# Optimization experiments

Measured on AMD Instinct MI355X. Metric: run time of the kernel, lower is better.

Reference implementation:

```python
import jax, jax.numpy as jnp
import numpy as np

# static module config (matches init_kwargs)
DIM = 128
HEADS = 8
DW, HW, WW = 5, 7, 7  # depth/height/width window


def _neighbor_indices(D, H, W):
    """Flat circular-neighborhood indices, shape (P, n) with P=D*H*W, n=DW*HW*WW."""
    od = np.arange(DW) - (DW - 1) // 2
    oh = np.arange(HW) - (HW - 1) // 2
    ow = np.arange(WW) - (WW - 1) // 2
    dd = (np.arange(D)[:, None] + od[None, :]) % D   # (D, DW)
    hh = (np.arange(H)[:, None] + oh[None, :]) % H   # (H, HW)
    ww = (np.arange(W)[:, None] + ow[None, :]) % W   # (W, WW)
    idx = (dd[:, None, None, :, None, None] * (H * W)
           + hh[None, :, None, None, :, None] * W
           + ww[None, None, :, None, None, :])        # (D,H,W,DW,HW,WW)
    return jnp.asarray(idx.reshape(D * H * W, DW * HW * WW), dtype=jnp.int32)


def setup_inputs() -> dict:
    key = jax.random.key(0)
    k1, k2, k3, k4, k5 = jax.random.split(key, 5)
    B, D, H, W, C = 1, 5, 24, 48, DIM
    w_scale = 1.0 / np.sqrt(C)  # keep attention logits in a sane range
    return {
        "x": jax.random.normal(k1, (B, D, H, W, C), dtype=jnp.float32),
        "qkv_w": jax.random.normal(k2, (3 * C, C), dtype=jnp.float32) * w_scale,
        "qkv_b": jax.random.normal(k3, (3 * C,), dtype=jnp.float32) * 0.01,
        "proj_w": jax.random.normal(k4, (C, C), dtype=jnp.float32) * w_scale,
        "proj_b": jax.random.normal(k5, (C,), dtype=jnp.float32) * 0.01,
    }


def reference(x, qkv_w, qkv_b, proj_w, proj_b):
    B, D, H, W, C = x.shape
    P = D * H * W
    n = DW * HW * WW
    hd = C // HEADS
    scale = hd ** -0.5
    idx = _neighbor_indices(D, H, W)                      # (P, n) int32, static

    xf = x.reshape(B, P, C)
    qkv = xf @ qkv_w.T + qkv_b                            # (B, P, 3C)
    q, k, v = jnp.split(qkv, 3, axis=-1)

    q = q.reshape(B, P, HEADS, hd)                        # center-pixel query
    k_g = k[:, idx].reshape(B, P, n, HEADS, hd)           # gathered circular neighborhood
    v_g = v[:, idx].reshape(B, P, n, HEADS, hd)

    scores = jnp.einsum('bphd,bpnhd->bhpn', q, k_g) * scale
    attn = jax.nn.softmax(scores, axis=-1)                # softmax over 245 neighbors
    out = jnp.einsum('bhpn,bpnhd->bphd', attn, v_g).reshape(B, P, C)
    out = out @ proj_w.T + proj_b
    return out.reshape(B, D, H, W, C)
```

## Files before the change

kernel.cpp:

```cpp
#include <hip/hip_runtime.h>
#include <hip/hip_bf16.h>
#include <cstddef>

#define DIMC   128
#define NHEADS 8
#define HDIM   16
#define DD     5
#define HH     24
#define WW_    48
#define NPOS   (DD * HH * WW_)
#define SCALE  0.25f

typedef short  bf16x8 __attribute__((ext_vector_type(8)));
typedef float  f32x4  __attribute__((ext_vector_type(4)));

__device__ __forceinline__ unsigned short f2bf(float f) {
    unsigned u = __float_as_uint(f);
    u = (u + 0x7FFFu + ((u >> 16) & 1u)) >> 16;
    return (unsigned short)u;
}
__device__ __forceinline__ float bf2f(unsigned short s) {
    return __uint_as_float(((unsigned)s) << 16);
}

__global__ __launch_bounds__(256, 3) void gemm_qkv_kernel(
    const float* __restrict__ x,
    const float* __restrict__ wq,
    const float* __restrict__ qkv_b,
    unsigned short* __restrict__ Qhl,
    unsigned short* __restrict__ Kbf,
    unsigned short* __restrict__ Vbf)
{
    __shared__ __align__(16) unsigned short Bs[64][264];

    const int tid = threadIdx.x;
    const int bn  = blockIdx.x * 64;
    const int bm  = blockIdx.y * 64;

    for (int i = tid; i < 2048; i += 256) {
        const int r = i >> 5, c4 = (i & 31) * 4;
        const float4 v = *(const float4*)(wq + (size_t)(bn + r) * 128 + c4);
        ushort4 hi, lo;
        hi.x = f2bf(v.x); hi.y = f2bf(v.y); hi.z = f2bf(v.z); hi.w = f2bf(v.w);
        lo.x = f2bf(v.x - bf2f(hi.x));
        lo.y = f2bf(v.y - bf2f(hi.y));
        lo.z = f2bf(v.z - bf2f(hi.z));
        lo.w = f2bf(v.w - bf2f(hi.w));
        *(ushort4*)(&Bs[r][c4])       = hi;
        *(ushort4*)(&Bs[r][128 + c4]) = lo;
    }
    __syncthreads();

    const int w    = tid >> 6;
    const int lane = tid & 63;
    const int ln   = lane & 15;
    const int quad = lane >> 4;
    const int row  = bm + w * 16 + ln;
    const float* ar = x + (size_t)row * 128 + quad * 8;

    f32x4 acc[4] = {};
    #pragma unroll
    for (int kcg = 0; kcg < 4; ++kcg) {
        const float4 xa = *(const float4*)(ar + kcg * 32);
        const float4 xb = *(const float4*)(ar + kcg * 32 + 4);
        bf16x8 ahi, alo;
        {
            const float vv[8] = {xa.x, xa.y, xa.z, xa.w, xb.x, xb.y, xb.z, xb.w};
            #pragma unroll
            for (int j = 0; j < 8; ++j) {
                const unsigned short hh = f2bf(vv[j]);
                ahi[j] = (short)hh;
                alo[j] = (short)f2bf(vv[j] - bf2f(hh));
            }
        }
        #pragma unroll
        for (int nt = 0; nt < 4; ++nt) {
            const bf16x8 bhi = *(const bf16x8*)(&Bs[nt * 16 + ln][kcg * 32 + quad * 8]);
            const bf16x8 blo = *(const bf16x8*)(&Bs[nt * 16 + ln][128 + kcg * 32 + quad * 8]);
            acc[nt] = __builtin_amdgcn_mfma_f32_16x16x32_bf16(ahi, bhi, acc[nt], 0, 0, 0);
            acc[nt] = __builtin_amdgcn_mfma_f32_16x16x32_bf16(alo, bhi, acc[nt], 0, 0, 0);
            acc[nt] = __builtin_amdgcn_mfma_f32_16x16x32_bf16(ahi, blo, acc[nt], 0, 0, 0);
        }
    }

    #pragma unroll
    for (int nt = 0; nt < 4; ++nt) {
        const int col = bn + nt * 16 + ln;
        const float bv = qkv_b[col];
        #pragma unroll
        for (int r = 0; r < 4; ++r) {
            const int orow = bm + w * 16 + quad * 4 + r;
            const float val = acc[nt][r] + bv;
            if (col < 128) {
                const int h = col >> 4, ci = col & 15;
                const unsigned short hi = f2bf(val);
                Qhl[(size_t)orow * 256 + h * 32 + ci]      = hi;
                Qhl[(size_t)orow * 256 + h * 32 + 16 + ci] = f2bf(val - bf2f(hi));
            } else if (col < 256) {
                Kbf[(size_t)orow * 128 + (col - 128)] = f2bf(val);
            } else {
                Vbf[(size_t)orow * 128 + (col - 256)] = f2bf(val);
            }
        }
    }
}

__global__ __launch_bounds__(128, 2) void gemm_proj_kernel(
    const unsigned short* __restrict__ Ap,
    const float* __restrict__ wp,
    const float* __restrict__ proj_b,
    float* __restrict__ out)
{
    __shared__ __align__(16) unsigned short Bs[64][264];

    const int tid = threadIdx.x;
    const int bn  = blockIdx.x * 64;
    const int bm  = blockIdx.y * 32;

    for (int i = tid; i < 2048; i += 128) {
        const int r = i >> 5, c4 = (i & 31) * 4;
        const float4 v = *(const float4*)(wp + (size_t)(bn + r) * 128 + c4);
        ushort4 hi, lo;
        hi.x = f2bf(v.x); hi.y = f2bf(v.y); hi.z = f2bf(v.z); hi.w = f2bf(v.w);
        lo.x = f2bf(v.x - bf2f(hi.x));
        lo.y = f2bf(v.y - bf2f(hi.y));
        lo.z = f2bf(v.z - bf2f(hi.z));
        lo.w = f2bf(v.w - bf2f(hi.w));
        *(ushort4*)(&Bs[r][c4])       = hi;
        *(ushort4*)(&Bs[r][128 + c4]) = lo;
    }
    __syncthreads();

    const int w    = tid >> 6;
    const int lane = tid & 63;
    const int ln   = lane & 15;
    const int quad = lane >> 4;
    const int row  = bm + w * 16 + ln;
    const unsigned short* ar = Ap + (size_t)row * 256 + quad * 8;

    f32x4 acc[4] = {};
    #pragma unroll
    for (int kcg = 0; kcg < 4; ++kcg) {
        const bf16x8 ahi = *(const bf16x8*)(ar + kcg * 32);
        const bf16x8 alo = *(const bf16x8*)(ar + 128 + kcg * 32);
        #pragma unroll
        for (int nt = 0; nt < 4; ++nt) {
            const bf16x8 bhi = *(const bf16x8*)(&Bs[nt * 16 + ln][kcg * 32 + quad * 8]);
            const bf16x8 blo = *(const bf16x8*)(&Bs[nt * 16 + ln][128 + kcg * 32 + quad * 8]);
            acc[nt] = __builtin_amdgcn_mfma_f32_16x16x32_bf16(ahi, bhi, acc[nt], 0, 0, 0);
            acc[nt] = __builtin_amdgcn_mfma_f32_16x16x32_bf16(alo, bhi, acc[nt], 0, 0, 0);
            acc[nt] = __builtin_amdgcn_mfma_f32_16x16x32_bf16(ahi, blo, acc[nt], 0, 0, 0);
        }
    }

    #pragma unroll
    for (int nt = 0; nt < 4; ++nt) {
        const int col = bn + nt * 16 + ln;
        const float bv = proj_b[col];
        #pragma unroll
        for (int r = 0; r < 4; ++r) {
            const int orow = bm + w * 16 + quad * 4 + r;
            out[(size_t)orow * 128 + col] = acc[nt][r] + bv;
        }
    }
}

__global__ __launch_bounds__(256, 3) void attn_kernel(
    const unsigned short* __restrict__ Qhl,
    const unsigned short* __restrict__ Kbf,
    const unsigned short* __restrict__ Vbf,
    unsigned short* __restrict__ Ap)
{
    __shared__ __align__(16) char smem[34560];
    unsigned short (*Vt)[520] = (unsigned short(*)[520])smem;
    unsigned short (*Qb)[40]  = (unsigned short(*)[40])(smem + 16640);
    unsigned short* PwBase    = (unsigned short*)(smem + 23040);
    float* red_l              = (float*)(smem + 33280);
    float* redO               = (float*)smem;

    const int tile = blockIdx.x;
    const int h    = blockIdx.y;
    const int ty0  = (tile / 12) * 4;
    const int tx0  = (tile % 12) * 4;
    const int tid  = threadIdx.x;

    for (int i = tid; i < 1024; i += 256) {
        const int u = i >> 1, half = i & 1;
        if (u < 500) {
            const int dp = u / 100;
            const int rr = u - dp * 100;
            const int yy = rr / 10;
            const int xx = rr - yy * 10;
            int y = ty0 - 3 + yy; if (y < 0) y += HH;  if (y >= HH) y -= HH;
            int x = tx0 - 3 + xx; if (x < 0) x += WW_; if (x >= WW_) x -= WW_;
            const int g = (dp * HH + y) * WW_ + x;
            const bf16x8 v = *(const bf16x8*)(Vbf + (size_t)g * 128 + h * 16 + half * 8);
            #pragma unroll
            for (int c = 0; c < 8; ++c) Vt[half * 8 + c][u] = (unsigned short)v[c];
        } else {
            #pragma unroll
            for (int c = 0; c < 8; ++c) Vt[half * 8 + c][u] = 0;
        }
    }
    for (int i = tid; i < 320; i += 256) {
        const int p = i >> 2, seg = i & 3;
        const int d = p >> 4, s = p & 15;
        const int sy = s >> 2, sx = s & 3;
        const int g = (d * HH + ty0 + sy) * WW_ + tx0 + sx;
        *(bf16x8*)(&Qb[p][seg * 8]) = *(const bf16x8*)(Qhl + (size_t)g * 256 + h * 32 + seg * 8);
    }
    __syncthreads();

    const int w    = tid >> 6;
    const int lane = tid & 63;
    const int ln   = lane & 15;
    const int quad = lane >> 4;
    const int sy   = ln >> 2, sx = ln & 3;

    unsigned short* Pw = PwBase + w * 1280;

    bf16x8 qf[5];
    #pragma unroll
    for (int mt = 0; mt < 5; ++mt)
        qf[mt] = *(const bf16x8*)(&Qb[mt * 16 + ln][quad * 8]);

    f32x4 Ow[5] = {};
    float lsum[5] = {};

    for (int chunk = 0; chunk < 4; ++chunk) {
        const int u0 = (w * 4 + chunk) * 32;

        int rowa, rowb;
        {
            const int ua = u0 + ln      < 500 ? u0 + ln      : 499;
            const int ub = u0 + 16 + ln < 500 ? u0 + 16 + ln : 499;
            int dp = ua / 100, rr = ua - dp * 100, yy = rr / 10, xx = rr - yy * 10;
            int y = ty0 - 3 + yy; if (y < 0) y += HH;  if (y >= HH) y -= HH;
            int x = tx0 - 3 + xx; if (x < 0) x += WW_; if (x >= WW_) x -= WW_;
            rowa = (dp * HH + y) * WW_ + x;
            dp = ub / 100; rr = ub - dp * 100; yy = rr / 10; xx = rr - yy * 10;
            y = ty0 - 3 + yy; if (y < 0) y += HH;  if (y >= HH) y -= HH;
            x = tx0 - 3 + xx; if (x < 0) x += WW_; if (x >= WW_) x -= WW_;
            rowb = (dp * HH + y) * WW_ + x;
        }
        const bf16x8 ka = *(const bf16x8*)(Kbf + (size_t)rowa * 128 + h * 16 + (quad & 1) * 8);
        const bf16x8 kb = *(const bf16x8*)(Kbf + (size_t)rowb * 128 + h * 16 + (quad & 1) * 8);

        bool msk[2][4];
        #pragma unroll
        for (int b = 0; b < 2; ++b)
            #pragma unroll
            for (int r = 0; r < 4; ++r) {
                const int u = u0 + 16 * b + 4 * quad + r;
                const int rr = u % 100;
                const int uy = rr / 10, ux = rr - uy * 10;
                msk[b][r] = (u < 500) && ((unsigned)(uy - sy) <= 6u)
                                      && ((unsigned)(ux - sx) <= 6u);
            }

        const bf16x8 vf = *(const bf16x8*)(&Vt[ln][u0 + quad * 8]);

        #pragma unroll
        for (int mt = 0; mt < 5; ++mt) {
            f32x4 s0 = __builtin_amdgcn_mfma_f32_16x16x32_bf16(
                ka, qf[mt], (f32x4){0.f, 0.f, 0.f, 0.f}, 0, 0, 0);
            f32x4 s1 = __builtin_amdgcn_mfma_f32_16x16x32_bf16(
                kb, qf[mt], (f32x4){0.f, 0.f, 0.f, 0.f}, 0, 0, 0);

            unsigned short* pw = Pw + (mt & 1) * 640 + ln * 40;
            #pragma unroll
            for (int b = 0; b < 2; ++b) {
                const f32x4 s = b ? s1 : s0;
                unsigned short e[4];
                #pragma unroll
                for (int r = 0; r < 4; ++r) {
                    const float ev = msk[b][r] ? __expf(fmaf(s[r], SCALE, -8.0f)) : 0.f;
                    e[r] = f2bf(ev);
                    lsum[mt] += bf2f(e[r]);
                }
                *(unsigned*)(pw + 16 * b + 4 * quad)     = (unsigned)e[0] | ((unsigned)e[1] << 16);
                *(unsigned*)(pw + 16 * b + 4 * quad + 2) = (unsigned)e[2] | ((unsigned)e[3] << 16);
            }
            const bf16x8 pf = *(const bf16x8*)(Pw + (mt & 1) * 640 + ln * 40 + quad * 8);
            Ow[mt] = __builtin_amdgcn_mfma_f32_16x16x32_bf16(vf, pf, Ow[mt], 0, 0, 0);
        }
    }

    #pragma unroll
    for (int mt = 0; mt < 5; ++mt) {
        lsum[mt] += __shfl_xor(lsum[mt], 16);
        lsum[mt] += __shfl_xor(lsum[mt], 32);
    }

    __syncthreads();

    if (quad == 0) {
        #pragma unroll
        for (int mt = 0; mt < 5; ++mt)
            red_l[w * 80 + mt * 16 + ln] = lsum[mt];
    }
    #pragma unroll
    for (int mt = 0; mt < 5; ++mt)
        #pragma unroll
        for (int r = 0; r < 4; ++r)
            redO[(size_t)((w * 5 + mt) * 16 + quad * 4 + r) * 16 + ln] = Ow[mt][r];
    __syncthreads();

    for (int i = tid; i < 1280; i += 256) {
        const int m = i >> 4, c = i & 15;
        const int mt = m >> 4, mloc = m & 15;
        float o = 0.f, l = 0.f;
        #pragma unroll
        for (int w4 = 0; w4 < 4; ++w4) {
            o += redO[(size_t)((w4 * 5 + mt) * 16 + c) * 16 + mloc];
            l += red_l[w4 * 80 + m];
        }
        const float val = o / l;
        const int qsy = (mloc >> 2), qsx = mloc & 3;
        const size_t g = (size_t)((mt * HH + ty0 + qsy) * WW_ + (tx0 + qsx));
        const unsigned short hi = f2bf(val);
        const unsigned short lo = f2bf(val - bf2f(hi));
        unsigned short* row = Ap + g * 256 + h * HDIM + c;
        row[0]   = hi;
        row[128] = lo;
    }
}

extern "C" void kernel_launch(void* const* d_in, const int* in_sizes, int n_in,
                              void* d_out, int out_size, void* d_ws, size_t ws_size,
                              hipStream_t stream)
{
    const float* x      = (const float*)d_in[0];
    const float* qkv_w  = (const float*)d_in[1];
    const float* qkv_b  = (const float*)d_in[2];
    const float* proj_w = (const float*)d_in[3];
    const float* proj_b = (const float*)d_in[4];
    float* out = (float*)d_out;

    char* ws = (char*)d_ws;
    unsigned short* Ap  = (unsigned short*)ws;  ws += (size_t)NPOS * 256 * 2;
    unsigned short* Qhl = (unsigned short*)ws;  ws += (size_t)NPOS * 256 * 2;
    unsigned short* Kbf = (unsigned short*)ws;  ws += (size_t)NPOS * 128 * 2;
    unsigned short* Vbf = (unsigned short*)ws;  ws += (size_t)NPOS * 128 * 2;

    {
        dim3 grid(384 / 64, NPOS / 64);
        gemm_qkv_kernel<<<grid, 256, 0, stream>>>(x, qkv_w, qkv_b, Qhl, Kbf, Vbf);
    }
    {
        dim3 grid(72, NHEADS);
        attn_kernel<<<grid, 256, 0, stream>>>(Qhl, Kbf, Vbf, Ap);
    }
    {
        dim3 grid(DIMC / 64, NPOS / 32);
        gemm_proj_kernel<<<grid, 128, 0, stream>>>(Ap, proj_w, proj_b, out);
    }
}
```

Measured before the change: 99.85 us.

## Split attention neighbor range across two blocks and merge partials in projection GEMM

The attention kernel now splits each tile's 500-slot neighbor range into two halves, each handled by its own block. This doubles the grid from 576 to 1152 blocks and halves the LDS footprint, so occupancy can rise. Each block writes unnormalized fp32 partial outputs and row sums; the projection GEMM adds the two partials, normalizes, and does the hi/lo bf16 split inline. The gain in parallelism on a small grid costs larger fp32 intermediate traffic (two partial buffers instead of one bf16 pair) and extra work in the projection kernel.

```diff
diff --git a/kernel.cpp b/kernel.cpp
--- a/kernel.cpp
+++ b/kernel.cpp
@@ -106,7 +106,8 @@
 }
 
 __global__ __launch_bounds__(128, 2) void gemm_proj_kernel(
-    const unsigned short* __restrict__ Ap,
+    const float* __restrict__ Opart,
+    const float* __restrict__ Lpart,
     const float* __restrict__ wp,
     const float* __restrict__ proj_b,
     float* __restrict__ out)
@@ -136,13 +137,41 @@
     const int ln   = lane & 15;
     const int quad = lane >> 4;
     const int row  = bm + w * 16 + ln;
-    const unsigned short* ar = Ap + (size_t)row * 256 + quad * 8;
+
+    float linv[8];
+    {
+        const float4 l0a = *(const float4*)(Lpart + (size_t)row * 8);
+        const float4 l0b = *(const float4*)(Lpart + (size_t)row * 8 + 4);
+        const float4 l1a = *(const float4*)(Lpart + (size_t)(NPOS + row) * 8);
+        const float4 l1b = *(const float4*)(Lpart + (size_t)(NPOS + row) * 8 + 4);
+        linv[0] = 1.0f / (l0a.x + l1a.x); linv[1] = 1.0f / (l0a.y + l1a.y);
+        linv[2] = 1.0f / (l0a.z + l1a.z); linv[3] = 1.0f / (l0a.w + l1a.w);
+        linv[4] = 1.0f / (l0b.x + l1b.x); linv[5] = 1.0f / (l0b.y + l1b.y);
+        linv[6] = 1.0f / (l0b.z + l1b.z); linv[7] = 1.0f / (l0b.w + l1b.w);
+    }
+    const float* o0 = Opart + (size_t)row * 128 + quad * 8;
+    const float* o1 = o0 + (size_t)NPOS * 128;
 
     f32x4 acc[4] = {};
     #pragma unroll
     for (int kcg = 0; kcg < 4; ++kcg) {
-        const bf16x8 ahi = *(const bf16x8*)(ar + kcg * 32);
-        const bf16x8 alo = *(const bf16x8*)(ar + 128 + kcg * 32);
+        const float4 a0 = *(const float4*)(o0 + kcg * 32);
+        const float4 a0b = *(const float4*)(o0 + kcg * 32 + 4);
+        const float4 a1 = *(const float4*)(o1 + kcg * 32);
+        const float4 a1b = *(const float4*)(o1 + kcg * 32 + 4);
+        const float inv = linv[kcg * 2 + (quad >> 1)];
+        const float vv[8] = {
+            (a0.x + a1.x) * inv, (a0.y + a1.y) * inv,
+            (a0.z + a1.z) * inv, (a0.w + a1.w) * inv,
+            (a0b.x + a1b.x) * inv, (a0b.y + a1b.y) * inv,
+            (a0b.z + a1b.z) * inv, (a0b.w + a1b.w) * inv };
+        bf16x8 ahi, alo;
+        #pragma unroll
+        for (int j = 0; j < 8; ++j) {
+            const unsigned short hh = f2bf(vv[j]);
+            ahi[j] = (short)hh;
+            alo[j] = (short)f2bf(vv[j] - bf2f(hh));
+        }
         #pragma unroll
         for (int nt = 0; nt < 4; ++nt) {
             const bf16x8 bhi = *(const bf16x8*)(&Bs[nt * 16 + ln][kcg * 32 + quad * 8]);
@@ -165,27 +194,31 @@
     }
 }
 
-__global__ __launch_bounds__(256, 3) void attn_kernel(
+__global__ __launch_bounds__(256, 4) void attn_kernel(
     const unsigned short* __restrict__ Qhl,
     const unsigned short* __restrict__ Kbf,
     const unsigned short* __restrict__ Vbf,
-    unsigned short* __restrict__ Ap)
+    float* __restrict__ Opart,
+    float* __restrict__ Lpart)
 {
-    __shared__ __align__(16) char smem[34560];
-    unsigned short (*Vt)[520] = (unsigned short(*)[520])smem;
-    unsigned short (*Qb)[40]  = (unsigned short(*)[40])(smem + 16640);
-    unsigned short* PwBase    = (unsigned short*)(smem + 23040);
-    float* red_l              = (float*)(smem + 33280);
+    __shared__ __align__(16) char smem[26368];
+    unsigned short (*Vt)[264] = (unsigned short(*)[264])smem;
+    unsigned short (*Qb)[40]  = (unsigned short(*)[40])(smem + 8448);
+    unsigned short* PwBase    = (unsigned short*)(smem + 14848);
+    float* red_l              = (float*)(smem + 25088);
     float* redO               = (float*)smem;
 
-    const int tile = blockIdx.x;
+    const int bx   = blockIdx.x;
+    const int tile = bx >> 1;
+    const int half = bx & 1;
     const int h    = blockIdx.y;
     const int ty0  = (tile / 12) * 4;
     const int tx0  = (tile % 12) * 4;
     const int tid  = threadIdx.x;
 
-    for (int i = tid; i < 1024; i += 256) {
-        const int u = i >> 1, half = i & 1;
+    for (int i = tid; i < 512; i += 256) {
+        const int ul = i >> 1, hf8 = i & 1;
+        const int u  = half * 256 + ul;
         if (u < 500) {
             const int dp = u / 100;
             const int rr = u - dp * 100;
@@ -194,12 +227,12 @@
             int y = ty0 - 3 + yy; if (y < 0) y += HH;  if (y >= HH) y -= HH;
             int x = tx0 - 3 + xx; if (x < 0) x += WW_; if (x >= WW_) x -= WW_;
             const int g = (dp * HH + y) * WW_ + x;
-            const bf16x8 v = *(const bf16x8*)(Vbf + (size_t)g * 128 + h * 16 + half * 8);
-            #pragma unroll
-            for (int c = 0; c < 8; ++c) Vt[half * 8 + c][u] = (unsigned short)v[c];
+            const bf16x8 v = *(const bf16x8*)(Vbf + (size_t)g * 128 + h * 16 + hf8 * 8);
+            #pragma unroll
+            for (int c = 0; c < 8; ++c) Vt[hf8 * 8 + c][ul] = (unsigned short)v[c];
         } else {
             #pragma unroll
-            for (int c = 0; c < 8; ++c) Vt[half * 8 + c][u] = 0;
+            for (int c = 0; c < 8; ++c) Vt[hf8 * 8 + c][ul] = 0;
         }
     }
     for (int i = tid; i < 320; i += 256) {
@@ -227,13 +260,15 @@
     f32x4 Ow[5] = {};
     float lsum[5] = {};
 
-    for (int chunk = 0; chunk < 4; ++chunk) {
-        const int u0 = (w * 4 + chunk) * 32;
+    #pragma unroll
+    for (int chunk = 0; chunk < 2; ++chunk) {
+        const int u0g = (half * 8 + w * 2 + chunk) * 32;
+        const int u0l = (w * 2 + chunk) * 32;
 
         int rowa, rowb;
         {
-            const int ua = u0 + ln      < 500 ? u0 + ln      : 499;
-            const int ub = u0 + 16 + ln < 500 ? u0 + 16 + ln : 499;
+            const int ua = u0g + ln      < 500 ? u0g + ln      : 499;
+            const int ub = u0g + 16 + ln < 500 ? u0g + 16 + ln : 499;
             int dp = ua / 100, rr = ua - dp * 100, yy = rr / 10, xx = rr - yy * 10;
             int y = ty0 - 3 + yy; if (y < 0) y += HH;  if (y >= HH) y -= HH;
             int x = tx0 - 3 + xx; if (x < 0) x += WW_; if (x >= WW_) x -= WW_;
@@ -251,14 +286,14 @@
         for (int b = 0; b < 2; ++b)
             #pragma unroll
             for (int r = 0; r < 4; ++r) {
-                const int u = u0 + 16 * b + 4 * quad + r;
+                const int u = u0g + 16 * b + 4 * quad + r;
                 const int rr = u % 100;
                 const int uy = rr / 10, ux = rr - uy * 10;
                 msk[b][r] = (u < 500) && ((unsigned)(uy - sy) <= 6u)
                                       && ((unsigned)(ux - sx) <= 6u);
             }
 
-        const bf16x8 vf = *(const bf16x8*)(&Vt[ln][u0 + quad * 8]);
+        const bf16x8 vf = *(const bf16x8*)(&Vt[ln][u0l + quad * 8]);
 
         #pragma unroll
         for (int mt = 0; mt < 5; ++mt) {
@@ -315,14 +350,10 @@
             o += redO[(size_t)((w4 * 5 + mt) * 16 + c) * 16 + mloc];
             l += red_l[w4 * 80 + m];
         }
-        const float val = o / l;
         const int qsy = (mloc >> 2), qsx = mloc & 3;
         const size_t g = (size_t)((mt * HH + ty0 + qsy) * WW_ + (tx0 + qsx));
-        const unsigned short hi = f2bf(val);
-        const unsigned short lo = f2bf(val - bf2f(hi));
-        unsigned short* row = Ap + g * 256 + h * HDIM + c;
-        row[0]   = hi;
-        row[128] = lo;
+        Opart[((size_t)half * NPOS + g) * 128 + h * HDIM + c] = o;
+        if (c == 0) Lpart[((size_t)half * NPOS + g) * 8 + h] = l;
     }
 }
 
@@ -338,21 +369,22 @@
     float* out = (float*)d_out;
 
     char* ws = (char*)d_ws;
-    unsigned short* Ap  = (unsigned short*)ws;  ws += (size_t)NPOS * 256 * 2;
-    unsigned short* Qhl = (unsigned short*)ws;  ws += (size_t)NPOS * 256 * 2;
-    unsigned short* Kbf = (unsigned short*)ws;  ws += (size_t)NPOS * 128 * 2;
-    unsigned short* Vbf = (unsigned short*)ws;  ws += (size_t)NPOS * 128 * 2;
+    unsigned short* Qhl   = (unsigned short*)ws;  ws += (size_t)NPOS * 256 * 2;
+    unsigned short* Kbf   = (unsigned short*)ws;  ws += (size_t)NPOS * 128 * 2;
+    unsigned short* Vbf   = (unsigned short*)ws;  ws += (size_t)NPOS * 128 * 2;
+    float*          Opart = (float*)ws;           ws += (size_t)2 * NPOS * 128 * 4;
+    float*          Lpart = (float*)ws;           ws += (size_t)2 * NPOS * 8 * 4;
 
     {
         dim3 grid(384 / 64, NPOS / 64);
         gemm_qkv_kernel<<<grid, 256, 0, stream>>>(x, qkv_w, qkv_b, Qhl, Kbf, Vbf);
     }
     {
-        dim3 grid(72, NHEADS);
-        attn_kernel<<<grid, 256, 0, stream>>>(Qhl, Kbf, Vbf, Ap);
+        dim3 grid(144, NHEADS);
+        attn_kernel<<<grid, 256, 0, stream>>>(Qhl, Kbf, Vbf, Opart, Lpart);
     }
     {
         dim3 grid(DIMC / 64, NPOS / 32);
-        gemm_proj_kernel<<<grid, 128, 0, stream>>>(Ap, proj_w, proj_b, out);
-    }
-}
+        gemm_proj_kernel<<<grid, 128, 0, stream>>>(Opart, Lpart, proj_w, proj_b, out);
+    }
+}
```

Measured after the change: 98.86 us (median of 2 runs). About the same (-1.0%).

## Fuse output projection into attention kernel via per-head atomic accumulation

Applied to the files above, without the earlier changes.

Removes the separate projection GEMM kernel and the Ap intermediate buffer. Each attention block multiplies its per-head 16-channel output by the matching 16-column slice of proj_w using MFMA and atomically adds into the output, with head 0 adding the bias. The output is zeroed inside the QKV GEMM kernel. This saves one launch and the Ap round trip through global memory, but adds 8-way float atomic contention per output element and makes the summation order nondeterministic.

```diff
diff --git a/kernel.cpp b/kernel.cpp
--- a/kernel.cpp
+++ b/kernel.cpp
@@ -29,13 +29,21 @@
     const float* __restrict__ qkv_b,
     unsigned short* __restrict__ Qhl,
     unsigned short* __restrict__ Kbf,
-    unsigned short* __restrict__ Vbf)
+    unsigned short* __restrict__ Vbf,
+    float* __restrict__ out)
 {
     __shared__ __align__(16) unsigned short Bs[64][264];
 
     const int tid = threadIdx.x;
     const int bn  = blockIdx.x * 64;
     const int bm  = blockIdx.y * 64;
+    const int bid = blockIdx.y * 6 + blockIdx.x;
+
+    {
+        float4* o4 = (float4*)out;
+        const float4 z = make_float4(0.f, 0.f, 0.f, 0.f);
+        for (int i = bid * 256 + tid; i < 184320; i += 540 * 256) o4[i] = z;
+    }
 
     for (int i = tid; i < 2048; i += 256) {
         const int r = i >> 5, c4 = (i & 31) * 4;
@@ -105,78 +113,22 @@
     }
 }
 
-__global__ __launch_bounds__(128, 2) void gemm_proj_kernel(
-    const unsigned short* __restrict__ Ap,
+__global__ __launch_bounds__(256, 3) void attn_proj_kernel(
+    const unsigned short* __restrict__ Qhl,
+    const unsigned short* __restrict__ Kbf,
+    const unsigned short* __restrict__ Vbf,
     const float* __restrict__ wp,
     const float* __restrict__ proj_b,
     float* __restrict__ out)
 {
-    __shared__ __align__(16) unsigned short Bs[64][264];
-
-    const int tid = threadIdx.x;
-    const int bn  = blockIdx.x * 64;
-    const int bm  = blockIdx.y * 32;
-
-    for (int i = tid; i < 2048; i += 128) {
-        const int r = i >> 5, c4 = (i & 31) * 4;
-        const float4 v = *(const float4*)(wp + (size_t)(bn + r) * 128 + c4);
-        ushort4 hi, lo;
-        hi.x = f2bf(v.x); hi.y = f2bf(v.y); hi.z = f2bf(v.z); hi.w = f2bf(v.w);
-        lo.x = f2bf(v.x - bf2f(hi.x));
-        lo.y = f2bf(v.y - bf2f(hi.y));
-        lo.z = f2bf(v.z - bf2f(hi.z));
-        lo.w = f2bf(v.w - bf2f(hi.w));
-        *(ushort4*)(&Bs[r][c4])       = hi;
-        *(ushort4*)(&Bs[r][128 + c4]) = lo;
-    }
-    __syncthreads();
-
-    const int w    = tid >> 6;
-    const int lane = tid & 63;
-    const int ln   = lane & 15;
-    const int quad = lane >> 4;
-    const int row  = bm + w * 16 + ln;
-    const unsigned short* ar = Ap + (size_t)row * 256 + quad * 8;
-
-    f32x4 acc[4] = {};
-    #pragma unroll
-    for (int kcg = 0; kcg < 4; ++kcg) {
-        const bf16x8 ahi = *(const bf16x8*)(ar + kcg * 32);
-        const bf16x8 alo = *(const bf16x8*)(ar + 128 + kcg * 32);
-        #pragma unroll
-        for (int nt = 0; nt < 4; ++nt) {
-            const bf16x8 bhi = *(const bf16x8*)(&Bs[nt * 16 + ln][kcg * 32 + quad * 8]);
-            const bf16x8 blo = *(const bf16x8*)(&Bs[nt * 16 + ln][128 + kcg * 32 + quad * 8]);
-            acc[nt] = __builtin_amdgcn_mfma_f32_16x16x32_bf16(ahi, bhi, acc[nt], 0, 0, 0);
-            acc[nt] = __builtin_amdgcn_mfma_f32_16x16x32_bf16(alo, bhi, acc[nt], 0, 0, 0);
-            acc[nt] = __builtin_amdgcn_mfma_f32_16x16x32_bf16(ahi, blo, acc[nt], 0, 0, 0);
-        }
-    }
-
-    #pragma unroll
-    for (int nt = 0; nt < 4; ++nt) {
-        const int col = bn + nt * 16 + ln;
-        const float bv = proj_b[col];
-        #pragma unroll
-        for (int r = 0; r < 4; ++r) {
-            const int orow = bm + w * 16 + quad * 4 + r;
-            out[(size_t)orow * 128 + col] = acc[nt][r] + bv;
-        }
-    }
-}
-
-__global__ __launch_bounds__(256, 3) void attn_kernel(
-    const unsigned short* __restrict__ Qhl,
-    const unsigned short* __restrict__ Kbf,
-    const unsigned short* __restrict__ Vbf,
-    unsigned short* __restrict__ Ap)
-{
-    __shared__ __align__(16) char smem[34560];
+    __shared__ __align__(16) char smem[35072];
     unsigned short (*Vt)[520] = (unsigned short(*)[520])smem;
     unsigned short (*Qb)[40]  = (unsigned short(*)[40])(smem + 16640);
     unsigned short* PwBase    = (unsigned short*)(smem + 23040);
-    float* red_l              = (float*)(smem + 33280);
+    float* red_l              = (float*)(smem + 33792);
     float* redO               = (float*)smem;
+    unsigned short* Wb        = (unsigned short*)(smem + 20480);
+    unsigned short* Ahl       = (unsigned short*)(smem + 28672);
 
     const int tile = blockIdx.x;
     const int h    = blockIdx.y;
@@ -304,6 +256,13 @@
         #pragma unroll
         for (int r = 0; r < 4; ++r)
             redO[(size_t)((w * 5 + mt) * 16 + quad * 4 + r) * 16 + ln] = Ow[mt][r];
+    for (int i = tid; i < 2048; i += 256) {
+        const int n = i >> 4, kk = i & 15;
+        const float v = wp[(size_t)n * 128 + h * 16 + kk];
+        const unsigned short hi = f2bf(v);
+        Wb[n * 32 + kk]      = hi;
+        Wb[n * 32 + 16 + kk] = f2bf(v - bf2f(hi));
+    }
     __syncthreads();
 
     for (int i = tid; i < 1280; i += 256) {
@@ -316,13 +275,28 @@
             l += red_l[w4 * 80 + m];
         }
         const float val = o / l;
-        const int qsy = (mloc >> 2), qsx = mloc & 3;
-        const size_t g = (size_t)((mt * HH + ty0 + qsy) * WW_ + (tx0 + qsx));
         const unsigned short hi = f2bf(val);
-        const unsigned short lo = f2bf(val - bf2f(hi));
-        unsigned short* row = Ap + g * 256 + h * HDIM + c;
-        row[0]   = hi;
-        row[128] = lo;
+        Ahl[m * 32 + c]      = hi;
+        Ahl[m * 32 + 16 + c] = f2bf(val - bf2f(hi));
+    }
+    __syncthreads();
+
+    for (int t = w; t < 40; t += 4) {
+        const int mt = t >> 3, nt = t & 7;
+        const unsigned short* am = Ahl + (mt * 16 + ln) * 32;
+        const bf16x8 a1 = *(const bf16x8*)(am + (quad & 1) * 8);
+        bf16x8 a2 = {0, 0, 0, 0, 0, 0, 0, 0};
+        if (quad < 2) a2 = *(const bf16x8*)(am + 16 + quad * 8);
+        const bf16x8 b = *(const bf16x8*)(Wb + (nt * 16 + ln) * 32 + quad * 8);
+        f32x4 acc = __builtin_amdgcn_mfma_f32_16x16x32_bf16(a1, b, (f32x4){0.f,0.f,0.f,0.f}, 0, 0, 0);
+        acc = __builtin_amdgcn_mfma_f32_16x16x32_bf16(a2, b, acc, 0, 0, 0);
+        const int col = nt * 16 + ln;
+        const float bias = (h == 0) ? proj_b[col] : 0.f;
+        #pragma unroll
+        for (int r = 0; r < 4; ++r) {
+            const size_t g = (size_t)((mt * HH + ty0 + quad) * WW_ + (tx0 + r));
+            atomicAdd(&out[g * 128 + col], acc[r] + bias);
+        }
     }
 }
 
@@ -338,21 +312,16 @@
     float* out = (float*)d_out;
 
     char* ws = (char*)d_ws;
-    unsigned short* Ap  = (unsigned short*)ws;  ws += (size_t)NPOS * 256 * 2;
     unsigned short* Qhl = (unsigned short*)ws;  ws += (size_t)NPOS * 256 * 2;
     unsigned short* Kbf = (unsigned short*)ws;  ws += (size_t)NPOS * 128 * 2;
     unsigned short* Vbf = (unsigned short*)ws;  ws += (size_t)NPOS * 128 * 2;
 
     {
         dim3 grid(384 / 64, NPOS / 64);
-        gemm_qkv_kernel<<<grid, 256, 0, stream>>>(x, qkv_w, qkv_b, Qhl, Kbf, Vbf);
+        gemm_qkv_kernel<<<grid, 256, 0, stream>>>(x, qkv_w, qkv_b, Qhl, Kbf, Vbf, out);
     }
     {
         dim3 grid(72, NHEADS);
-        attn_kernel<<<grid, 256, 0, stream>>>(Qhl, Kbf, Vbf, Ap);
-    }
-    {
-        dim3 grid(DIMC / 64, NPOS / 32);
-        gemm_proj_kernel<<<grid, 128, 0, stream>>>(Ap, proj_w, proj_b, out);
-    }
-}
+        attn_proj_kernel<<<grid, 256, 0, stream>>>(Qhl, Kbf, Vbf, proj_w, proj_b, out);
+    }
+}
```

After: 104.5 us. +4.6%, slower.
